# Performance work log

Hardware: AMD Instinct MI355X
Metric: run time of the kernel (lower is better)

The kernel has to match this reference:

```python
import jax, jax.numpy as jnp
import numpy as np

D = 1024  # input_size
H = 1024  # hidden_size
B = 128
R = 512


def _lin(x, W, b):
    return x @ W + b


def setup_inputs() -> dict:
    key = jax.random.key(0)
    ks = jax.random.split(key, 20)
    s = 0.02
    inp = {
        "V": jax.random.normal(ks[0], (B, R, D), jnp.float32),
        "s_t": jax.random.normal(ks[1], (B, D), jnp.float32),
        "h_t": jax.random.normal(ks[2], (B, D), jnp.float32),
        # weights stored [in, out] (y = x @ W + b)
        "Wv": jax.random.normal(ks[3], (D, H), jnp.float32) * s,
        "bv": jnp.zeros((H,), jnp.float32),
        "Wsp": jax.random.normal(ks[4], (D, D), jnp.float32) * s,
        "bsp": jnp.zeros((D,), jnp.float32),
        "Wsa": jax.random.normal(ks[5], (D, H), jnp.float32) * s,
        "bsa": jnp.zeros((H,), jnp.float32),
        "Whp": jax.random.normal(ks[6], (D, D), jnp.float32) * s,
        "bhp": jnp.zeros((D,), jnp.float32),
        "Wha": jax.random.normal(ks[7], (D, H), jnp.float32) * s,
        "bha": jnp.zeros((H,), jnp.float32),
        "Wal": jax.random.normal(ks[8], (H, 1), jnp.float32) * s,
        "bal": jnp.zeros((1,), jnp.float32),
        "Wcp": jax.random.normal(ks[9], (D, D), jnp.float32) * s,
        "bcp": jnp.zeros((D,), jnp.float32),
    }
    return inp


def reference(V, s_t, h_t, Wv, bv, Wsp, bsp, Wsa, bsa, Whp, bhp, Wha, bha, Wal, bal, Wcp, bcp):
    v_embed = jax.nn.relu(_lin(V, Wv, bv))           # [B,R,H]
    s_proj = jax.nn.relu(_lin(s_t, Wsp, bsp))        # [B,D]
    s_att = _lin(s_proj, Wsa, bsa)                   # [B,H]
    h_proj = jnp.tanh(_lin(h_t, Whp, bhp))           # [B,D]
    h_att = _lin(h_proj, Wha, bha)                   # [B,H]
    regions = jnp.concatenate([V, s_proj[:, None, :]], axis=1)           # [B,R+1,D]
    regions_att = jnp.concatenate([v_embed, s_att[:, None, :]], axis=1)  # [B,R+1,H]
    alpha_input = jnp.tanh(regions_att + h_att[:, None, :])              # [B,R+1,H]
    scores = (_lin(alpha_input, Wal, bal)).squeeze(-1)                   # [B,R+1]
    alpha = jax.nn.softmax(scores, axis=1)                               # [B,R+1]
    context = jnp.einsum("br,brd->bd", alpha, regions)                   # [B,D]
    z_t = jnp.tanh(_lin(context + h_proj, Wcp, bcp))                     # [B,D]
    return z_t
```

## Files before the change

kernel.cpp:

```cpp
#include <hip/hip_runtime.h>


typedef __bf16 bf16x8 __attribute__((ext_vector_type(8)));
typedef float floatx4 __attribute__((ext_vector_type(4)));

__device__ __forceinline__ float tanh_fast(float x) {
    x = fminf(10.0f, fmaxf(-10.0f, x));
    float e = exp2f(x * 2.885390081777927f);
    return (e - 1.0f) * __builtin_amdgcn_rcpf(e + 1.0f);
}

__global__ __launch_bounds__(256) void conv_k(
    const float* __restrict__ V, __bf16* __restrict__ Vb) {
    const size_t i = ((size_t)blockIdx.x * 256 + threadIdx.x) * 8;
    const float4 a = *reinterpret_cast<const float4*>(V + i);
    const float4 b = *reinterpret_cast<const float4*>(V + i + 4);
    bf16x8 o;
    o[0] = (__bf16)a.x; o[1] = (__bf16)a.y;
    o[2] = (__bf16)a.z; o[3] = (__bf16)a.w;
    o[4] = (__bf16)b.x; o[5] = (__bf16)b.y;
    o[6] = (__bf16)b.z; o[7] = (__bf16)b.w;
    *reinterpret_cast<bf16x8*>(Vb + i) = o;
}

__global__ __launch_bounds__(256) void wvt_kernel(
    const float* __restrict__ Wv, __bf16* __restrict__ WvT) {
    __shared__ float tile[64][65];
    const int k0 = blockIdx.x * 64, n0 = blockIdx.y * 64;
    const int c = threadIdx.x & 63, r = threadIdx.x >> 6;
#pragma unroll
    for (int i = 0; i < 16; ++i)
        tile[r + i * 4][c] = Wv[(size_t)(k0 + r + i * 4) * 1024 + n0 + c];
    __syncthreads();
#pragma unroll
    for (int i = 0; i < 16; ++i)
        WvT[(size_t)(n0 + r + i * 4) * 1024 + k0 + c] =
            (__bf16)tile[c][r + i * 4];
}

__global__ __launch_bounds__(512) void small_gemm_k(
    const float* __restrict__ A0, const float* __restrict__ W0,
    const float* __restrict__ b0, float* __restrict__ C0, int act0,
    const float* __restrict__ A1, const float* __restrict__ W1,
    const float* __restrict__ b1, float* __restrict__ C1, int act1) {
    const float* A; const float* W; const float* bs; float* C; int act;
    if (blockIdx.z == 0) { A = A0; W = W0; bs = b0; C = C0; act = act0; }
    else                 { A = A1; W = W1; bs = b1; C = C1; act = act1; }
    __shared__ float red[3][8][128];
    const int tid = threadIdx.x;
    const int nl = tid & 127, kq = tid >> 7;
    const int n = blockIdx.x * 128 + nl;
    const int m0 = blockIdx.y * 8;
    const float* Ab = A + m0 * 1024;
    float acc[8] = {};
    const int kbeg = kq * 256, kend = kbeg + 256;
#pragma unroll 4
    for (int k = kbeg; k < kend; ++k) {
        float w = W[(size_t)k * 1024 + n];
#pragma unroll
        for (int mi = 0; mi < 8; ++mi)
            acc[mi] = fmaf(Ab[mi * 1024 + k], w, acc[mi]);
    }
    if (kq > 0) {
#pragma unroll
        for (int mi = 0; mi < 8; ++mi) red[kq - 1][mi][nl] = acc[mi];
    }
    __syncthreads();
    if (kq == 0) {
        float bias = bs[n];
#pragma unroll
        for (int mi = 0; mi < 8; ++mi) {
            float v = acc[mi] + red[0][mi][nl] + red[1][mi][nl] +
                      red[2][mi][nl] + bias;
            if (act == 1) v = fmaxf(v, 0.0f);
            else if (act == 2) v = tanh_fast(v);
            C[(size_t)(m0 + mi) * 1024 + n] = v;
        }
    }
}

__global__ __launch_bounds__(512, 2) void score_gemm_k(
    const __bf16* __restrict__ Vb, const __bf16* __restrict__ WvT,
    const float* __restrict__ bv, const float* __restrict__ h_att,
    const float* __restrict__ Wal, float* __restrict__ scores) {
    __shared__ __bf16 As[2][128 * 32];
    __shared__ __bf16 Bs[2][256 * 32];

    const int tid = threadIdx.x;
    const int bid = blockIdx.x;
    const int xcd = bid & 7;
    const int j = bid >> 3;
    const int mtile = xcd * 64 + (j >> 2);
    const int ntile = j & 3;
    const int m0 = mtile * 128, n0 = ntile * 256;
    const int wid = tid >> 6, lane = tid & 63;
    const int wm = wid & 1, wn = wid >> 1;
    const int lcol = lane & 15, quad = lane >> 4;

    floatx4 acc[4][4] = {};

    const int grow = tid >> 2;
    const int kg = (tid & 3) ^ ((tid >> 3) & 3);
    const __bf16* ap0 = Vb + (size_t)(m0 + grow) * 1024 + kg * 8;
    const __bf16* bp0 = WvT + (size_t)(n0 + grow) * 1024 + kg * 8;

    auto dma = [&](int buf, int k0) {
        __builtin_amdgcn_global_load_lds(
            (const __attribute__((address_space(1))) void*)(ap0 + k0),
            (__attribute__((address_space(3))) void*)(&As[buf][tid * 8]),
            16, 0, 0);
        __builtin_amdgcn_global_load_lds(
            (const __attribute__((address_space(1))) void*)(bp0 + k0),
            (__attribute__((address_space(3))) void*)(&Bs[buf][tid * 8]),
            16, 0, 0);
        __builtin_amdgcn_global_load_lds(
            (const __attribute__((address_space(1))) void*)(bp0 + 128 * 1024 + k0),
            (__attribute__((address_space(3))) void*)(&Bs[buf][(512 + tid) * 8]),
            16, 0, 0);
    };

    int aoff[4], boff[4];
#pragma unroll
    for (int i = 0; i < 4; ++i) {
        int r = wm * 64 + i * 16 + lcol;
        aoff[i] = r * 32 + ((quad ^ ((r >> 1) & 3)) * 8);
        int n = wn * 64 + i * 16 + lcol;
        boff[i] = n * 32 + ((quad ^ ((n >> 1) & 3)) * 8);
    }

    dma(0, 0);
    __syncthreads();

    for (int kk = 0; kk < 32; ++kk) {
        const int cur = kk & 1;
        if (kk < 31) dma(cur ^ 1, (kk + 1) * 32);
        bf16x8 af[4], bfr[4];
#pragma unroll
        for (int i = 0; i < 4; ++i) {
            af[i] = *reinterpret_cast<const bf16x8*>(&As[cur][aoff[i]]);
            bfr[i] = *reinterpret_cast<const bf16x8*>(&Bs[cur][boff[i]]);
        }
#pragma unroll
        for (int mi = 0; mi < 4; ++mi)
#pragma unroll
            for (int ni = 0; ni < 4; ++ni)
                acc[mi][ni] = __builtin_amdgcn_mfma_f32_16x16x32_bf16(
                    af[mi], bfr[ni], acc[mi][ni], 0, 0, 0);
        __syncthreads();
    }

    const int b = m0 >> 9;
    float wal[4], hat[4], bvv[4];
#pragma unroll
    for (int ni = 0; ni < 4; ++ni) {
        int n = n0 + wn * 64 + ni * 16 + lcol;
        wal[ni] = Wal[n];
        hat[ni] = h_att[b * 1024 + n];
        bvv[ni] = bv[n];
    }
    float p[16];
#pragma unroll
    for (int mi = 0; mi < 4; ++mi) {
#pragma unroll
        for (int rg = 0; rg < 4; ++rg) {
            float s = 0.f;
#pragma unroll
            for (int ni = 0; ni < 4; ++ni) {
                float x = acc[mi][ni][rg] + bvv[ni];
                x = fmaxf(x, 0.f);
                s = fmaf(wal[ni], tanh_fast(x + hat[ni]), s);
            }
            p[mi * 4 + rg] = s;
        }
    }
#pragma unroll
    for (int off = 1; off < 16; off <<= 1) {
#pragma unroll
        for (int i = 0; i < 16; ++i) p[i] += __shfl_xor(p[i], off, 64);
    }
    if (lcol == 0) {
#pragma unroll
        for (int mi = 0; mi < 4; ++mi)
#pragma unroll
            for (int rg = 0; rg < 4; ++rg) {
                int row = m0 + wm * 64 + mi * 16 + quad * 4 + rg;
                atomicAdd(&scores[b * 513 + (row & 511)], p[mi * 4 + rg]);
            }
    }
}

__global__ __launch_bounds__(256, 3) void score_gemm_fb(
    const float* __restrict__ V, const __bf16* __restrict__ WvT,
    const float* __restrict__ bv, const float* __restrict__ h_att,
    const float* __restrict__ Wal, float* __restrict__ scores) {
    __shared__ __bf16 As[2][128 * 40];
    __shared__ __bf16 Bs[2][128 * 32];

    const int tid = threadIdx.x;
    const int bid = blockIdx.x;
    const int xcd = bid & 7;
    const int j = bid >> 3;
    const int mtile = xcd * 64 + (j >> 3);
    const int ntile = j & 7;
    const int m0 = mtile * 128, n0 = ntile * 128;
    const int wid = tid >> 6, lane = tid & 63;
    const int wm = wid & 1, wn = wid >> 1;
    const int lcol = lane & 15, quad = lane >> 4;

    floatx4 acc[4][4] = {};

    const int am = tid >> 1;
    const int ak = (tid & 1) * 16;
    const float* aptr = V + (size_t)(m0 + am) * 1024 + ak;

    const int g0n = tid >> 2, g0ks = tid & 3;
    const int g1n = (256 + tid) >> 2, g1ks = tid & 3;
    const int g0kg = g0ks ^ ((g0n >> 1) & 3);
    const int g1kg = g1ks ^ ((g1n >> 1) & 3);
    const __bf16* bp0 = WvT + (size_t)(n0 + g0n) * 1024 + g0kg * 8;
    const __bf16* bp1 = WvT + (size_t)(n0 + g1n) * 1024 + g1kg * 8;

    auto stage_A = [&](int buf, float4 f0, float4 f1, float4 f2, float4 f3) {
        bf16x8 u0, u1;
        u0[0] = (__bf16)f0.x; u0[1] = (__bf16)f0.y;
        u0[2] = (__bf16)f0.z; u0[3] = (__bf16)f0.w;
        u0[4] = (__bf16)f1.x; u0[5] = (__bf16)f1.y;
        u0[6] = (__bf16)f1.z; u0[7] = (__bf16)f1.w;
        u1[0] = (__bf16)f2.x; u1[1] = (__bf16)f2.y;
        u1[2] = (__bf16)f2.z; u1[3] = (__bf16)f2.w;
        u1[4] = (__bf16)f3.x; u1[5] = (__bf16)f3.y;
        u1[6] = (__bf16)f3.z; u1[7] = (__bf16)f3.w;
        __bf16* awr = &As[buf][am * 40 + ak];
        *reinterpret_cast<bf16x8*>(awr) = u0;
        *reinterpret_cast<bf16x8*>(awr + 8) = u1;
    };
    auto dma_B = [&](int buf, int k0) {
        __builtin_amdgcn_global_load_lds(
            (const __attribute__((address_space(1))) void*)(bp0 + k0),
            (__attribute__((address_space(3))) void*)(&Bs[buf][tid * 8]),
            16, 0, 0);
        __builtin_amdgcn_global_load_lds(
            (const __attribute__((address_space(1))) void*)(bp1 + k0),
            (__attribute__((address_space(3))) void*)(&Bs[buf][(256 + tid) * 8]),
            16, 0, 0);
    };

    dma_B(0, 0);
    {
        const float4* fp = reinterpret_cast<const float4*>(aptr);
        stage_A(0, fp[0], fp[1], fp[2], fp[3]);
    }
    __syncthreads();

    for (int kk = 0; kk < 32; ++kk) {
        const int cur = kk & 1, nxt = cur ^ 1;
        float4 f0, f1, f2, f3;
        const bool pf = (kk < 31);
        if (pf) {
            dma_B(nxt, (kk + 1) * 32);
            const float4* fp =
                reinterpret_cast<const float4*>(aptr + (kk + 1) * 32);
            f0 = fp[0]; f1 = fp[1]; f2 = fp[2]; f3 = fp[3];
        }
        bf16x8 af[4], bfr[4];
#pragma unroll
        for (int mi = 0; mi < 4; ++mi)
            af[mi] = *reinterpret_cast<const bf16x8*>(
                &As[cur][(wm * 64 + mi * 16 + lcol) * 40 + quad * 8]);
#pragma unroll
        for (int ni = 0; ni < 4; ++ni) {
            int n = wn * 64 + ni * 16 + lcol;
            int ks = quad ^ ((n >> 1) & 3);
            bfr[ni] = *reinterpret_cast<const bf16x8*>(
                &Bs[cur][n * 32 + ks * 8]);
        }
#pragma unroll
        for (int mi = 0; mi < 4; ++mi)
#pragma unroll
            for (int ni = 0; ni < 4; ++ni)
                acc[mi][ni] = __builtin_amdgcn_mfma_f32_16x16x32_bf16(
                    af[mi], bfr[ni], acc[mi][ni], 0, 0, 0);
        if (pf) stage_A(nxt, f0, f1, f2, f3);
        __syncthreads();
    }

    const int b = m0 >> 9;
    float wal[4], hat[4], bvv[4];
#pragma unroll
    for (int ni = 0; ni < 4; ++ni) {
        int n = n0 + wn * 64 + ni * 16 + lcol;
        wal[ni] = Wal[n];
        hat[ni] = h_att[b * 1024 + n];
        bvv[ni] = bv[n];
    }
    float p[16];
#pragma unroll
    for (int mi = 0; mi < 4; ++mi) {
#pragma unroll
        for (int rg = 0; rg < 4; ++rg) {
            float s = 0.f;
#pragma unroll
            for (int ni = 0; ni < 4; ++ni) {
                float x = acc[mi][ni][rg] + bvv[ni];
                x = fmaxf(x, 0.f);
                s = fmaf(wal[ni], tanh_fast(x + hat[ni]), s);
            }
            p[mi * 4 + rg] = s;
        }
    }
#pragma unroll
    for (int off = 1; off < 16; off <<= 1) {
#pragma unroll
        for (int i = 0; i < 16; ++i) p[i] += __shfl_xor(p[i], off, 64);
    }
    if (lcol == 0) {
#pragma unroll
        for (int mi = 0; mi < 4; ++mi)
#pragma unroll
            for (int rg = 0; rg < 4; ++rg) {
                int row = m0 + wm * 64 + mi * 16 + quad * 4 + rg;
                atomicAdd(&scores[b * 513 + (row & 511)], p[mi * 4 + rg]);
            }
    }
}

__global__ __launch_bounds__(256) void lastrow_k(
    const float* __restrict__ s_att, const float* __restrict__ h_att,
    const float* __restrict__ Wal, float* __restrict__ scores) {
    int b = blockIdx.x, tid = threadIdx.x;
    float s = 0.f;
    for (int h = tid; h < 1024; h += 256)
        s += Wal[h] * tanh_fast(s_att[b * 1024 + h] + h_att[b * 1024 + h]);
#pragma unroll
    for (int off = 32; off >= 1; off >>= 1) s += __shfl_xor(s, off, 64);
    __shared__ float red[4];
    if ((tid & 63) == 0) red[tid >> 6] = s;
    __syncthreads();
    if (tid == 0) scores[b * 513 + 512] = red[0] + red[1] + red[2] + red[3];
}

__global__ __launch_bounds__(256) void softmax_k(
    const float* __restrict__ scores, float* __restrict__ alpha) {
    int b = blockIdx.x, tid = threadIdx.x;
    const float* s = scores + b * 513;
    float v0 = s[tid];
    float v1 = s[tid + 256];
    float v2 = (tid == 0) ? s[512] : -1e30f;
    float m = fmaxf(v0, fmaxf(v1, v2));
#pragma unroll
    for (int off = 32; off >= 1; off >>= 1) m = fmaxf(m, __shfl_xor(m, off, 64));
    __shared__ float red[4];
    int w = tid >> 6;
    if ((tid & 63) == 0) red[w] = m;
    __syncthreads();
    m = fmaxf(fmaxf(red[0], red[1]), fmaxf(red[2], red[3]));
    const float L2E = 1.4426950408889634f;
    float e0 = exp2f((v0 - m) * L2E);
    float e1 = exp2f((v1 - m) * L2E);
    float e2 = (tid == 0) ? exp2f((v2 - m) * L2E) : 0.f;
    float sum = e0 + e1 + e2;
#pragma unroll
    for (int off = 32; off >= 1; off >>= 1) sum += __shfl_xor(sum, off, 64);
    __syncthreads();
    if ((tid & 63) == 0) red[w] = sum;
    __syncthreads();
    sum = red[0] + red[1] + red[2] + red[3];
    float inv = 1.0f / sum;
    float* a = alpha + b * 513;
    a[tid] = e0 * inv;
    a[tid + 256] = e1 * inv;
    if (tid == 0) a[512] = e2 * inv;
}

__global__ __launch_bounds__(256) void ctx_k(
    const __bf16* __restrict__ Vb, const float* __restrict__ alpha,
    const float* __restrict__ s_proj, const float* __restrict__ h_proj,
    float* __restrict__ ctxsum) {
    const int b = blockIdx.x, dq = blockIdx.y;
    const int tid = threadIdx.x;
    const int dl = tid & 63, rq = tid >> 6;
    __shared__ float sal[513];
    __shared__ float red[3][64][9];
    for (int i = tid; i < 513; i += 256) sal[i] = alpha[b * 513 + i];
    __syncthreads();
    const int d0 = dq * 512 + dl * 8;
    const __bf16* vp = Vb + ((size_t)b * 512 + rq * 128) * 1024 + d0;
    float a[8] = {};
#pragma unroll 4
    for (int r = 0; r < 128; ++r) {
        float al = sal[rq * 128 + r];
        bf16x8 vv = *reinterpret_cast<const bf16x8*>(vp + (size_t)r * 1024);
#pragma unroll
        for (int jj = 0; jj < 8; ++jj) a[jj] = fmaf(al, (float)vv[jj], a[jj]);
    }
    if (rq > 0) {
#pragma unroll
        for (int jj = 0; jj < 8; ++jj) red[rq - 1][dl][jj] = a[jj];
    }
    __syncthreads();
    if (rq == 0) {
#pragma unroll
        for (int q = 0; q < 3; ++q)
#pragma unroll
            for (int jj = 0; jj < 8; ++jj) a[jj] += red[q][dl][jj];
        float aR = sal[512];
        float4 sp0 = *reinterpret_cast<const float4*>(s_proj + b * 1024 + d0);
        float4 sp1 = *reinterpret_cast<const float4*>(s_proj + b * 1024 + d0 + 4);
        float4 hp0 = *reinterpret_cast<const float4*>(h_proj + b * 1024 + d0);
        float4 hp1 = *reinterpret_cast<const float4*>(h_proj + b * 1024 + d0 + 4);
        float4 o0, o1;
        o0.x = fmaf(aR, sp0.x, a[0]) + hp0.x;
        o0.y = fmaf(aR, sp0.y, a[1]) + hp0.y;
        o0.z = fmaf(aR, sp0.z, a[2]) + hp0.z;
        o0.w = fmaf(aR, sp0.w, a[3]) + hp0.w;
        o1.x = fmaf(aR, sp1.x, a[4]) + hp1.x;
        o1.y = fmaf(aR, sp1.y, a[5]) + hp1.y;
        o1.z = fmaf(aR, sp1.z, a[6]) + hp1.z;
        o1.w = fmaf(aR, sp1.w, a[7]) + hp1.w;
        *reinterpret_cast<float4*>(ctxsum + b * 1024 + d0) = o0;
        *reinterpret_cast<float4*>(ctxsum + b * 1024 + d0 + 4) = o1;
    }
}

__global__ __launch_bounds__(256) void ctx_fb(
    const float* __restrict__ V, const float* __restrict__ alpha,
    const float* __restrict__ s_proj, const float* __restrict__ h_proj,
    float* __restrict__ ctxsum) {
    const int b = blockIdx.x, dq = blockIdx.y;
    const int tid = threadIdx.x;
    const int dl = tid & 63, rq = tid >> 6;
    __shared__ float sal[513];
    __shared__ float red[3][64][4];
    for (int i = tid; i < 513; i += 256) sal[i] = alpha[b * 513 + i];
    __syncthreads();
    const int d0 = dq * 256 + dl * 4;
    const float* vp = V + ((size_t)b * 512 + rq * 128) * 1024 + d0;
    float a0 = 0, a1 = 0, a2 = 0, a3 = 0;
#pragma unroll 8
    for (int r = 0; r < 128; ++r) {
        float al = sal[rq * 128 + r];
        const float4 vv = *reinterpret_cast<const float4*>(vp + (size_t)r * 1024);
        a0 = fmaf(al, vv.x, a0); a1 = fmaf(al, vv.y, a1);
        a2 = fmaf(al, vv.z, a2); a3 = fmaf(al, vv.w, a3);
    }
    if (rq > 0) {
        red[rq - 1][dl][0] = a0; red[rq - 1][dl][1] = a1;
        red[rq - 1][dl][2] = a2; red[rq - 1][dl][3] = a3;
    }
    __syncthreads();
    if (rq == 0) {
#pragma unroll
        for (int q = 0; q < 3; ++q) {
            a0 += red[q][dl][0]; a1 += red[q][dl][1];
            a2 += red[q][dl][2]; a3 += red[q][dl][3];
        }
        float4 sp = *reinterpret_cast<const float4*>(s_proj + b * 1024 + d0);
        float4 hp = *reinterpret_cast<const float4*>(h_proj + b * 1024 + d0);
        float aR = sal[512];
        float4 o;
        o.x = fmaf(aR, sp.x, a0) + hp.x;
        o.y = fmaf(aR, sp.y, a1) + hp.y;
        o.z = fmaf(aR, sp.z, a2) + hp.z;
        o.w = fmaf(aR, sp.w, a3) + hp.w;
        *reinterpret_cast<float4*>(ctxsum + b * 1024 + d0) = o;
    }
}

extern "C" void kernel_launch(void* const* d_in, const int* in_sizes, int n_in,
                              void* d_out, int out_size, void* d_ws,
                              size_t ws_size, hipStream_t stream) {
    const float* V   = (const float*)d_in[0];
    const float* s_t = (const float*)d_in[1];
    const float* h_t = (const float*)d_in[2];
    const float* Wv  = (const float*)d_in[3];
    const float* bv  = (const float*)d_in[4];
    const float* Wsp = (const float*)d_in[5];
    const float* bsp = (const float*)d_in[6];
    const float* Wsa = (const float*)d_in[7];
    const float* bsa = (const float*)d_in[8];
    const float* Whp = (const float*)d_in[9];
    const float* bhp = (const float*)d_in[10];
    const float* Wha = (const float*)d_in[11];
    const float* bha = (const float*)d_in[12];
    const float* Wal = (const float*)d_in[13];
    const float* Wcp = (const float*)d_in[15];
    const float* bcp = (const float*)d_in[16];
    float* out = (float*)d_out;

    const size_t VB_BYTES = (size_t)128 * 512 * 1024 * 2;
    const size_t SMALL_BYTES = 5242880 + 64;
    const bool big = ws_size >= VB_BYTES + SMALL_BYTES;

    char* ws = (char*)d_ws;
    __bf16* Vb = (__bf16*)ws;
    char* base = big ? (ws + VB_BYTES) : ws;
    __bf16* WvT   = (__bf16*)(base + 0);
    float* s_proj = (float*)(base + 2097152);
    float* h_proj = (float*)(base + 2621440);
    float* s_att  = (float*)(base + 3145728);
    float* h_att  = (float*)(base + 3670016);
    float* scores = (float*)(base + 4194304);
    float* alpha  = (float*)(base + 4456960);
    float* ctxsum = (float*)(base + 4719616);

    if (big)
        hipLaunchKernelGGL(conv_k, dim3(32768), dim3(256), 0, stream, V, Vb);
    hipLaunchKernelGGL(wvt_kernel, dim3(16, 16), dim3(256), 0, stream, Wv, WvT);
    hipLaunchKernelGGL(small_gemm_k, dim3(8, 16, 2), dim3(512), 0, stream,
                       s_t, Wsp, bsp, s_proj, 1,
                       h_t, Whp, bhp, h_proj, 2);
    hipLaunchKernelGGL(small_gemm_k, dim3(8, 16, 2), dim3(512), 0, stream,
                       s_proj, Wsa, bsa, s_att, 0,
                       h_proj, Wha, bha, h_att, 0);
    (void)hipMemsetAsync(scores, 0, 128 * 513 * sizeof(float), stream);
    if (big)
        hipLaunchKernelGGL(score_gemm_k, dim3(2048), dim3(512), 0, stream,
                           Vb, WvT, bv, h_att, Wal, scores);
    else
        hipLaunchKernelGGL(score_gemm_fb, dim3(4096), dim3(256), 0, stream,
                           V, WvT, bv, h_att, Wal, scores);
    hipLaunchKernelGGL(lastrow_k, dim3(128), dim3(256), 0, stream,
                       s_att, h_att, Wal, scores);
    hipLaunchKernelGGL(softmax_k, dim3(128), dim3(256), 0, stream,
                       scores, alpha);
    if (big)
        hipLaunchKernelGGL(ctx_k, dim3(128, 2), dim3(256), 0, stream,
                           Vb, alpha, s_proj, h_proj, ctxsum);
    else
        hipLaunchKernelGGL(ctx_fb, dim3(128, 4), dim3(256), 0, stream,
                           V, alpha, s_proj, h_proj, ctxsum);
    hipLaunchKernelGGL(small_gemm_k, dim3(8, 16, 1), dim3(512), 0, stream,
                       ctxsum, Wcp, bcp, out, 2,
                       ctxsum, Wcp, bcp, out, 2);
}
```

Baseline: 786.3 us.

## Enlarge score GEMM tile to 256x256 with staged prefetch and interleaved LDS/MFMA schedule

The score GEMM tile grows from 128x256 to 256x256, which halves the grid and doubles each wave's accumulators. The main loop now processes K in 64-wide steps split into two 32-wide halves, with explicit vmcnt/lgkmcnt waits and raw s_barrier calls. DMA for the next stage is interleaved between MFMA groups, and s_setprio is raised around the MFMA bursts. The aim is more reuse of each B fragment and better overlap of global-to-LDS copies with matrix math. In exchange, occupancy drops to one block per CU, register pressure rises, and the hand-placed waitcnt counts risk subtle races.

Measured after the change: 775.6 us. Within noise of the previous version (-1.4%).

```diff
diff --git a/kernel.cpp b/kernel.cpp
--- a/kernel.cpp
+++ b/kernel.cpp
@@ -79,75 +79,135 @@
     }
 }
 
-__global__ __launch_bounds__(512, 2) void score_gemm_k(
+__global__ __launch_bounds__(512, 1) void score_gemm_k(
     const __bf16* __restrict__ Vb, const __bf16* __restrict__ WvT,
     const float* __restrict__ bv, const float* __restrict__ h_att,
     const float* __restrict__ Wal, float* __restrict__ scores) {
-    __shared__ __bf16 As[2][128 * 32];
-    __shared__ __bf16 Bs[2][256 * 32];
+    __shared__ __bf16 As[32768];
+    __shared__ __bf16 Bs[32768];
 
     const int tid = threadIdx.x;
     const int bid = blockIdx.x;
     const int xcd = bid & 7;
     const int j = bid >> 3;
-    const int mtile = xcd * 64 + (j >> 2);
+    const int mtile = xcd * 32 + (j >> 2);
     const int ntile = j & 3;
-    const int m0 = mtile * 128, n0 = ntile * 256;
+    const int m0 = mtile * 256, n0 = ntile * 256;
     const int wid = tid >> 6, lane = tid & 63;
     const int wm = wid & 1, wn = wid >> 1;
     const int lcol = lane & 15, quad = lane >> 4;
 
-    floatx4 acc[4][4] = {};
+    floatx4 acc[8][4] = {};
 
     const int grow = tid >> 2;
     const int kg = (tid & 3) ^ ((tid >> 3) & 3);
-    const __bf16* ap0 = Vb + (size_t)(m0 + grow) * 1024 + kg * 8;
-    const __bf16* bp0 = WvT + (size_t)(n0 + grow) * 1024 + kg * 8;
-
-    auto dma = [&](int buf, int k0) {
+    const __bf16* apA = Vb + (size_t)(m0 + grow) * 1024 + kg * 8;
+    const __bf16* apB = WvT + (size_t)(n0 + grow) * 1024 + kg * 8;
+
+    auto dmaA = [&](int nb, int ks, int k0) {
+        const __bf16* s = apA + k0 + ks * 32;
+        __bf16* d = &As[(nb * 2 + ks) * 8192 + tid * 8];
         __builtin_amdgcn_global_load_lds(
-            (const __attribute__((address_space(1))) void*)(ap0 + k0),
-            (__attribute__((address_space(3))) void*)(&As[buf][tid * 8]),
-            16, 0, 0);
+            (const __attribute__((address_space(1))) void*)s,
+            (__attribute__((address_space(3))) void*)d, 16, 0, 0);
         __builtin_amdgcn_global_load_lds(
-            (const __attribute__((address_space(1))) void*)(bp0 + k0),
-            (__attribute__((address_space(3))) void*)(&Bs[buf][tid * 8]),
-            16, 0, 0);
+            (const __attribute__((address_space(1))) void*)(s + 128 * 1024),
+            (__attribute__((address_space(3))) void*)(d + 4096), 16, 0, 0);
+    };
+    auto dmaB = [&](int nb, int ks, int k0) {
+        const __bf16* s = apB + k0 + ks * 32;
+        __bf16* d = &Bs[(nb * 2 + ks) * 8192 + tid * 8];
         __builtin_amdgcn_global_load_lds(
-            (const __attribute__((address_space(1))) void*)(bp0 + 128 * 1024 + k0),
-            (__attribute__((address_space(3))) void*)(&Bs[buf][(512 + tid) * 8]),
-            16, 0, 0);
+            (const __attribute__((address_space(1))) void*)s,
+            (__attribute__((address_space(3))) void*)d, 16, 0, 0);
+        __builtin_amdgcn_global_load_lds(
+            (const __attribute__((address_space(1))) void*)(s + 128 * 1024),
+            (__attribute__((address_space(3))) void*)(d + 4096), 16, 0, 0);
     };
 
-    int aoff[4], boff[4];
+    int aoff[8], boff[4];
+#pragma unroll
+    for (int i = 0; i < 8; ++i) {
+        int r = wm * 128 + i * 16 + lcol;
+        aoff[i] = r * 32 + ((quad ^ ((r >> 1) & 3)) * 8);
+    }
 #pragma unroll
     for (int i = 0; i < 4; ++i) {
-        int r = wm * 64 + i * 16 + lcol;
-        aoff[i] = r * 32 + ((quad ^ ((r >> 1) & 3)) * 8);
         int n = wn * 64 + i * 16 + lcol;
         boff[i] = n * 32 + ((quad ^ ((n >> 1) & 3)) * 8);
     }
 
-    dma(0, 0);
-    __syncthreads();
-
-    for (int kk = 0; kk < 32; ++kk) {
-        const int cur = kk & 1;
-        if (kk < 31) dma(cur ^ 1, (kk + 1) * 32);
-        bf16x8 af[4], bfr[4];
-#pragma unroll
-        for (int i = 0; i < 4; ++i) {
-            af[i] = *reinterpret_cast<const bf16x8*>(&As[cur][aoff[i]]);
-            bfr[i] = *reinterpret_cast<const bf16x8*>(&Bs[cur][boff[i]]);
-        }
-#pragma unroll
-        for (int mi = 0; mi < 4; ++mi)
-#pragma unroll
-            for (int ni = 0; ni < 4; ++ni)
-                acc[mi][ni] = __builtin_amdgcn_mfma_f32_16x16x32_bf16(
-                    af[mi], bfr[ni], acc[mi][ni], 0, 0, 0);
-        __syncthreads();
-    }
+    dmaA(0, 0, 0);
+    dmaB(0, 0, 0);
+    dmaA(0, 1, 0);
+    dmaB(0, 1, 0);
+
+#define LD_A(dst, base, i) \
+    dst = *reinterpret_cast<const bf16x8*>(&As[(base) + aoff[i]])
+#define LD_B(dst, base, i) \
+    dst = *reinterpret_cast<const bf16x8*>(&Bs[(base) + boff[i]])
+#define MFMA16(M0)                                                        \
+    __builtin_amdgcn_s_setprio(1);                                        \
+    _Pragma("unroll") for (int ni = 0; ni < 4; ++ni) {                    \
+        acc[M0 + 0][ni] = __builtin_amdgcn_mfma_f32_16x16x32_bf16(        \
+            a0, bf[ni], acc[M0 + 0][ni], 0, 0, 0);                        \
+        acc[M0 + 1][ni] = __builtin_amdgcn_mfma_f32_16x16x32_bf16(        \
+            a1, bf[ni], acc[M0 + 1][ni], 0, 0, 0);                        \
+        acc[M0 + 2][ni] = __builtin_amdgcn_mfma_f32_16x16x32_bf16(        \
+            a2, bf[ni], acc[M0 + 2][ni], 0, 0, 0);                        \
+        acc[M0 + 3][ni] = __builtin_amdgcn_mfma_f32_16x16x32_bf16(        \
+            a3, bf[ni], acc[M0 + 3][ni], 0, 0, 0);                        \
+    }                                                                     \
+    __builtin_amdgcn_s_setprio(0);
+
+#pragma unroll 2
+    for (int t = 0; t < 16; ++t) {
+        const int buf = t & 1, nbuf = buf ^ 1;
+        const int kn = ((t < 15) ? (t + 1) : 15) * 64;
+        const int asb0 = (buf * 2) * 8192, asb1 = asb0 + 8192;
+        bf16x8 a0, a1, a2, a3, bf[4];
+
+        asm volatile("s_waitcnt vmcnt(4)" ::: "memory");
+        LD_A(a0, asb0, 0); LD_A(a1, asb0, 1);
+        LD_A(a2, asb0, 2); LD_A(a3, asb0, 3);
+        LD_B(bf[0], asb0, 0); LD_B(bf[1], asb0, 1);
+        LD_B(bf[2], asb0, 2); LD_B(bf[3], asb0, 3);
+        dmaA(nbuf, 0, kn);
+        __builtin_amdgcn_s_barrier();
+        asm volatile("s_waitcnt lgkmcnt(0)" ::: "memory");
+        MFMA16(0)
+        __builtin_amdgcn_s_barrier();
+
+        LD_A(a0, asb0, 4); LD_A(a1, asb0, 5);
+        LD_A(a2, asb0, 6); LD_A(a3, asb0, 7);
+        dmaB(nbuf, 0, kn);
+        __builtin_amdgcn_s_barrier();
+        asm volatile("s_waitcnt lgkmcnt(0)" ::: "memory");
+        MFMA16(4)
+        __builtin_amdgcn_s_barrier();
+
+        asm volatile("s_waitcnt vmcnt(4)" ::: "memory");
+        LD_A(a0, asb1, 0); LD_A(a1, asb1, 1);
+        LD_A(a2, asb1, 2); LD_A(a3, asb1, 3);
+        LD_B(bf[0], asb1, 0); LD_B(bf[1], asb1, 1);
+        LD_B(bf[2], asb1, 2); LD_B(bf[3], asb1, 3);
+        dmaA(nbuf, 1, kn);
+        __builtin_amdgcn_s_barrier();
+        asm volatile("s_waitcnt lgkmcnt(0)" ::: "memory");
+        MFMA16(0)
+        __builtin_amdgcn_s_barrier();
+
+        LD_A(a0, asb1, 4); LD_A(a1, asb1, 5);
+        LD_A(a2, asb1, 6); LD_A(a3, asb1, 7);
+        dmaB(nbuf, 1, kn);
+        __builtin_amdgcn_s_barrier();
+        asm volatile("s_waitcnt lgkmcnt(0)" ::: "memory");
+        MFMA16(4)
+        __builtin_amdgcn_s_barrier();
+    }
+#undef LD_A
+#undef LD_B
+#undef MFMA16
 
     const int b = m0 >> 9;
     float wal[4], hat[4], bvv[4];
@@ -158,9 +218,9 @@
         hat[ni] = h_att[b * 1024 + n];
         bvv[ni] = bv[n];
     }
-    float p[16];
-#pragma unroll
-    for (int mi = 0; mi < 4; ++mi) {
+    float p[32];
+#pragma unroll
+    for (int mi = 0; mi < 8; ++mi) {
 #pragma unroll
         for (int rg = 0; rg < 4; ++rg) {
             float s = 0.f;
@@ -176,14 +236,14 @@
 #pragma unroll
     for (int off = 1; off < 16; off <<= 1) {
 #pragma unroll
-        for (int i = 0; i < 16; ++i) p[i] += __shfl_xor(p[i], off, 64);
+        for (int i = 0; i < 32; ++i) p[i] += __shfl_xor(p[i], off, 64);
     }
     if (lcol == 0) {
 #pragma unroll
-        for (int mi = 0; mi < 4; ++mi)
+        for (int mi = 0; mi < 8; ++mi)
 #pragma unroll
             for (int rg = 0; rg < 4; ++rg) {
-                int row = m0 + wm * 64 + mi * 16 + quad * 4 + rg;
+                int row = m0 + wm * 128 + mi * 16 + quad * 4 + rg;
                 atomicAdd(&scores[b * 513 + (row & 511)], p[mi * 4 + rg]);
             }
     }
@@ -514,7 +574,7 @@
                        h_proj, Wha, bha, h_att, 0);
     (void)hipMemsetAsync(scores, 0, 128 * 513 * sizeof(float), stream);
     if (big)
-        hipLaunchKernelGGL(score_gemm_k, dim3(2048), dim3(512), 0, stream,
+        hipLaunchKernelGGL(score_gemm_k, dim3(1024), dim3(512), 0, stream,
                            Vb, WvT, bv, h_att, Wal, scores);
     else
         hipLaunchKernelGGL(score_gemm_fb, dim3(4096), dim3(256), 0, stream,
```
